# Performance work log

Measured on AMD Instinct MI355X. Metric: run time of the kernel, lower is better.

## Reference

```python
import jax, jax.numpy as jnp
import numpy as np

L, H, NH, KVH, HD, F, P, DLM, N = 4, 1024, 16, 2, 64, 4096, 4, 2048, 8192
QLEN = P + 1  # patch_size + 1 (special token prepended)
EPS = 1e-5


def _rms(x, w):
    return x * jax.lax.rsqrt(jnp.mean(x * x, axis=-1, keepdims=True) + EPS) * w


def _rotate_half(x):
    x1, x2 = jnp.split(x, 2, axis=-1)  # split_size = head_dim // 2
    return jnp.concatenate([-x2, x1], axis=-1)


def _rope_tables():
    pos = jnp.arange(QLEN, dtype=jnp.float32)
    inv_freq = 1.0 / (10000.0 ** (jnp.arange(0, HD, 2, dtype=jnp.float32) / HD))
    freqs = pos[:, None] * inv_freq[None, :]
    emb = jnp.concatenate([freqs, freqs], axis=-1)  # [QLEN, HD]
    scale = HD ** -0.25  # scale_factor baked into cos/sin as in source
    return jnp.cos(emb) * scale, jnp.sin(emb) * scale


def setup_inputs() -> dict:
    key = jax.random.key(0)
    ks = jax.random.split(key, 12)
    s = 0.02
    return {
        "audio_feat": jax.random.normal(ks[0], (N, P, 64), jnp.float32),
        "special_token": jax.random.normal(ks[1], (H,), jnp.float32) * s,
        "in_proj_w": jax.random.normal(ks[2], (64, H), jnp.float32) * s,
        "ln1_w": jnp.ones((L, H), jnp.float32),
        "wq": jax.random.normal(ks[3], (L, H, NH * HD), jnp.float32) * s,
        "wk": jax.random.normal(ks[4], (L, H, KVH * HD), jnp.float32) * s,
        "wv": jax.random.normal(ks[5], (L, H, KVH * HD), jnp.float32) * s,
        "wo": jax.random.normal(ks[6], (L, NH * HD, H), jnp.float32) * s,
        "ln2_w": jnp.ones((L, H), jnp.float32),
        "w_gate": jax.random.normal(ks[7], (L, H, F), jnp.float32) * s,
        "w_up": jax.random.normal(ks[8], (L, H, F), jnp.float32) * s,
        "w_down": jax.random.normal(ks[9], (L, F, H), jnp.float32) * s,
        "final_norm_w": jnp.ones((H,), jnp.float32),
        "enc_to_lm_w": jax.random.normal(ks[10], (H, DLM), jnp.float32) * s,
    }


def reference(audio_feat, special_token, in_proj_w, ln1_w, wq, wk, wv, wo,
              ln2_w, w_gate, w_up, w_down, final_norm_w, enc_to_lm_w):
    n = audio_feat.shape[0]
    h = audio_feat @ in_proj_w  # [N, P, H]
    sp = jnp.broadcast_to(special_token, (n, 1, H))
    h = jnp.concatenate([sp, h], axis=1)  # [N, QLEN, H]
    cos, sin = _rope_tables()
    g = NH // KVH  # num_key_value_groups
    for l in range(L):
        x = _rms(h, ln1_w[l])
        q = (x @ wq[l]).reshape(n, QLEN, NH, HD).transpose(0, 2, 1, 3)
        k = (x @ wk[l]).reshape(n, QLEN, KVH, HD).transpose(0, 2, 1, 3)
        v = (x @ wv[l]).reshape(n, QLEN, KVH, HD).transpose(0, 2, 1, 3)
        q = q * cos + _rotate_half(q) * sin
        k = k * cos + _rotate_half(k) * sin
        # explicit GQA repeat (cat-then-view == repeat along head axis)
        k = jnp.repeat(k, g, axis=1)
        v = jnp.repeat(v, g, axis=1)
        attn = jax.nn.softmax(jnp.einsum('bhqd,bhkd->bhqk', q, k), axis=-1)
        ao = jnp.einsum('bhqk,bhkd->bhqd', attn, v)
        ao = ao.transpose(0, 2, 1, 3).reshape(n, QLEN, NH * HD)
        h = h + ao @ wo[l]
        r = h
        x = _rms(h, ln2_w[l])
        h = r + (jax.nn.silu(x @ w_gate[l]) * (x @ w_up[l])) @ w_down[l]
    feat = _rms(h[:, 0], final_norm_w) @ enc_to_lm_w  # [N, DLM]
    return feat[None]  # [1, N, DLM]
```

## Files before the change

### kernel.cpp

```cpp
#include <hip/hip_runtime.h>
#include <hip/hip_bf16.h>

#define NSAMP 8192
#define QL 5
#define MTOK (NSAMP*QL)

typedef __hip_bfloat16 bf16;
typedef __attribute__((ext_vector_type(8))) __bf16 bf16x8;
typedef __attribute__((ext_vector_type(8))) unsigned short u16x8;
typedef __attribute__((ext_vector_type(4))) float f32x4;

__device__ __forceinline__ float bfu2f(unsigned short u){ return __uint_as_float(((unsigned)u)<<16); }
__device__ __forceinline__ float bf2f(bf16 v){ return __bfloat162float(v); }
__device__ __forceinline__ bf16  f2bf(float v){ return __float2bfloat16(v); }
__device__ __forceinline__ unsigned short f2bfu(float v){
  __hip_bfloat16 b = __float2bfloat16(v);
  return __builtin_bit_cast(unsigned short, b);
}

__device__ __forceinline__ void gload16(const void* g, void* l){
  __builtin_amdgcn_global_load_lds(
      (const __attribute__((address_space(1))) unsigned int*)g,
      (__attribute__((address_space(3))) unsigned int*)l, 16, 0, 0);
}

__device__ __forceinline__ void transpose_body(const float* __restrict__ in,
                                               bf16* __restrict__ out,
                                               int K, int N, int nb, int kb, int rmap){
  __shared__ float tile[32][33];
  int tx = threadIdx.x, ty = threadIdx.y;
  #pragma unroll
  for (int j=0;j<4;j++)
    tile[ty+8*j][tx] = in[(size_t)(kb+ty+8*j)*N + nb+tx];
  __syncthreads();
  #pragma unroll
  for (int j=0;j<4;j++){
    int n = nb+ty+8*j;
    int R = (rmap==0) ? n : (((n>>4)<<5) + (n&15) + (rmap==2 ? 16 : 0));
    out[(size_t)R*K + kb+tx] = f2bf(tile[tx][ty+8*j]);
  }
}

__global__ __launch_bounds__(256) void k_transpose_cvt(const float* __restrict__ in,
                                                       bf16* __restrict__ out,
                                                       int K, int N){
  transpose_body(in, out, K, N, blockIdx.x*32, blockIdx.y*32, 0);
}

__global__ __launch_bounds__(256) void k_transpose_layer(
    const float* __restrict__ wq, const float* __restrict__ wk,
    const float* __restrict__ wv, const float* __restrict__ wo,
    const float* __restrict__ wg, const float* __restrict__ wu,
    const float* __restrict__ wd,
    bf16* __restrict__ wqkvT, bf16* __restrict__ woT,
    bf16* __restrict__ wguT, bf16* __restrict__ wdT){
  int id = blockIdx.x;
  const float* in; bf16* out; int K=1024, N=1024, nbx=32, rmap=0;
  if (id < 1024){ in=wq; out=wqkvT; }
  else if (id < 1152){ id-=1024; in=wk; out=wqkvT+(size_t)1024*1024; N=128; nbx=4; }
  else if (id < 1280){ id-=1152; in=wv; out=wqkvT+(size_t)1152*1024; N=128; nbx=4; }
  else if (id < 2304){ id-=1280; in=wo; out=woT; }
  else if (id < 6400){ id-=2304; in=wg; out=wguT; N=4096; nbx=128; rmap=1; }
  else if (id < 10496){ id-=6400; in=wu; out=wguT; N=4096; nbx=128; rmap=2; }
  else { id-=10496; in=wd; out=wdT; K=4096; N=1024; nbx=32; }
  transpose_body(in, out, K, N, (id % nbx)*32, (id / nbx)*32, rmap);
}

__global__ __launch_bounds__(256) void k_cvt_bf16(const float* __restrict__ in,
                                                  bf16* __restrict__ out, int n4){
  int i = blockIdx.x*blockDim.x + threadIdx.x;
  if (i < n4){
    float4 v = ((const float4*)in)[i];
    out[4*i+0]=f2bf(v.x); out[4*i+1]=f2bf(v.y);
    out[4*i+2]=f2bf(v.z); out[4*i+3]=f2bf(v.w);
  }
}

__global__ __launch_bounds__(256) void k_fill_special(const float* __restrict__ sp,
                                                      bf16* __restrict__ h){
  int i = blockIdx.x*blockDim.x + threadIdx.x;
  int n = i >> 10, c = i & 1023;
  h[(size_t)n*QL*1024 + c] = f2bf(sp[c]);
}

__global__ void k_rope_tab(float* __restrict__ ctab, float* __restrict__ stab){
  int i = threadIdx.x;
  int t = i >> 6, d = i & 63, j = d & 31;
  float invf = __expf(-((float)j/32.0f) * logf(10000.0f));
  float ang  = (float)t * invf;
  const float s = 0.35355339059327373f;
  ctab[i] = cosf(ang)*s;
  stab[i] = sinf(ang)*s;
}

__global__ __launch_bounds__(256) void k_rmsnorm(const bf16* __restrict__ in,
                                                 const float* __restrict__ w,
                                                 bf16* __restrict__ out,
                                                 int nrows, int in_stride){
  int row  = blockIdx.x*4 + (threadIdx.x>>6);
  int lane = threadIdx.x & 63;
  if (row >= nrows) return;
  const bf16* p = in + (size_t)row*in_stride;
  float f[16]; float ss = 0.f;
  #pragma unroll
  for (int i=0;i<2;i++){
    u16x8 v = *(const u16x8*)(p + i*512 + lane*8);
    #pragma unroll
    for (int j=0;j<8;j++){ float x = bfu2f(v[j]); f[i*8+j] = x; ss += x*x; }
  }
  #pragma unroll
  for (int off=32; off; off>>=1) ss += __shfl_xor(ss, off);
  float inv = rsqrtf(ss * (1.0f/1024.0f) + 1e-5f);
  const float4* w4 = (const float4*)w;
  bf16* op = out + (size_t)row*1024;
  #pragma unroll
  for (int i=0;i<2;i++){
    int c = i*512 + lane*8;
    float4 wa = w4[c/4], wb = w4[c/4 + 1];
    u16x8 o;
    o[0]=f2bfu(f[i*8+0]*inv*wa.x); o[1]=f2bfu(f[i*8+1]*inv*wa.y);
    o[2]=f2bfu(f[i*8+2]*inv*wa.z); o[3]=f2bfu(f[i*8+3]*inv*wa.w);
    o[4]=f2bfu(f[i*8+4]*inv*wb.x); o[5]=f2bfu(f[i*8+5]*inv*wb.y);
    o[6]=f2bfu(f[i*8+6]*inv*wb.z); o[7]=f2bfu(f[i*8+7]*inv*wb.w);
    *(u16x8*)(op + c) = o;
  }
}

__global__ __launch_bounds__(256) void k_addnorm(bf16* __restrict__ h,
                                                 const float* __restrict__ w,
                                                 const bf16* __restrict__ add,
                                                 bf16* __restrict__ out,
                                                 int nrows){
  int row  = blockIdx.x*4 + (threadIdx.x>>6);
  int lane = threadIdx.x & 63;
  if (row >= nrows) return;
  bf16* hp = h + (size_t)row*1024;
  const bf16* ap = add + (size_t)row*1024;
  float f[16]; float ss = 0.f;
  u16x8 hv[2], av[2];
  #pragma unroll
  for (int i=0;i<2;i++){
    hv[i] = *(const u16x8*)(hp + i*512 + lane*8);
    av[i] = *(const u16x8*)(ap + i*512 + lane*8);
  }
  #pragma unroll
  for (int i=0;i<2;i++)
    #pragma unroll
    for (int j=0;j<8;j++){
      float x = bfu2f(hv[i][j]) + bfu2f(av[i][j]);
      f[i*8+j] = x; ss += x*x;
    }
  #pragma unroll
  for (int i=0;i<2;i++){
    u16x8 o;
    #pragma unroll
    for (int j=0;j<8;j++) o[j] = f2bfu(f[i*8+j]);
    *(u16x8*)(hp + i*512 + lane*8) = o;
  }
  #pragma unroll
  for (int off=32; off; off>>=1) ss += __shfl_xor(ss, off);
  float inv = rsqrtf(ss * (1.0f/1024.0f) + 1e-5f);
  const float4* w4 = (const float4*)w;
  bf16* op = out + (size_t)row*1024;
  #pragma unroll
  for (int i=0;i<2;i++){
    int c = i*512 + lane*8;
    float4 wa = w4[c/4], wb = w4[c/4 + 1];
    u16x8 o;
    o[0]=f2bfu(f[i*8+0]*inv*wa.x); o[1]=f2bfu(f[i*8+1]*inv*wa.y);
    o[2]=f2bfu(f[i*8+2]*inv*wa.z); o[3]=f2bfu(f[i*8+3]*inv*wa.w);
    o[4]=f2bfu(f[i*8+4]*inv*wb.x); o[5]=f2bfu(f[i*8+5]*inv*wb.y);
    o[6]=f2bfu(f[i*8+6]*inv*wb.z); o[7]=f2bfu(f[i*8+7]*inv*wb.w);
    *(u16x8*)(op + c) = o;
  }
}

__global__ __launch_bounds__(256) void k_add(bf16* __restrict__ h,
                                             const bf16* __restrict__ d, int n8){
  int i = blockIdx.x*blockDim.x + threadIdx.x;
  if (i < n8){
    u16x8 a = *(const u16x8*)(h + (size_t)i*8);
    u16x8 b = *(const u16x8*)(d + (size_t)i*8);
    u16x8 o;
    #pragma unroll
    for (int j=0;j<8;j++) o[j] = f2bfu(bfu2f(a[j]) + bfu2f(b[j]));
    *(u16x8*)(h + (size_t)i*8) = o;
  }
}

template<int OUTMODE>
__device__ __forceinline__ void gemm256_impl(const bf16* __restrict__ A,
                                             const bf16* __restrict__ B,
                                             float* __restrict__ Cf,
                                             bf16* __restrict__ Cb,
                                             int M, int N, int K, int ldc){
  __shared__ bf16 lds[65536];
  char* ldsb = (char*)lds;
  const int tid  = threadIdx.x;
  const int wid  = tid >> 6, lane = tid & 63;
  const int wr   = wid >> 2, wc  = wid & 3;
  const int fr   = lane & 15, fq = lane >> 4;
  const int swz = (fr & 7) << 4;
  const int cs0 = (fq*16) ^ swz;
  const int cs1 = (fq*16 + 64) ^ swz;
  const int srcR = lane >> 3;
  const int srcC = ((lane & 7) ^ srcR) * 8;

  const int bm0 = blockIdx.x*256, bn0 = blockIdx.y*256;
  const bf16* gA = A + (size_t)bm0*K;
  const bf16* gB = B + (size_t)bn0*K;
  const int nt = K >> 6;

  const int aOff = (wr ? 16384 : 0);
  const int bOff = 32768 + ((wc>>1) ? 16384 : 0) + (wc&1)*8192;
  const char* aB0 = ldsb + aOff + fr*128 + cs0;
  const char* aB1 = ldsb + aOff + fr*128 + cs1;
  const char* bB0 = ldsb + bOff + fr*128 + cs0;
  const char* bB1 = ldsb + bOff + fr*128 + cs1;

  f32x4 acc[8][4] = {};
  bf16x8 aF[8][2], bF[4][2];

#define STAGE(p, t, h) {                                                        \
    const bf16* G_ = ((h) < 2) ? gA : gB;                                       \
    const int rb_ = ((h)&1) ? 128 : 0;                                          \
    const int k0_ = (t) << 6;                                                   \
    _Pragma("unroll")                                                           \
    for (int j_=0;j_<2;j_++){                                                   \
      int blk_ = j_*8 + wid;                                                    \
      gload16(G_ + (size_t)(rb_ + blk_*8 + srcR)*K + k0_ + srcC,               \
              ldsb + (p)*65536 + (h)*16384 + blk_*1024);                        \
    }                                                                           \
  }
#define RD_A(p, m0_) {                                                          \
    _Pragma("unroll")                                                           \
    for (int m_=0;m_<4;m_++)                                                    \
      _Pragma("unroll")                                                         \
      for (int ks_=0;ks_<2;ks_++)                                               \
        aF[(m0_)+m_][ks_] = *(const bf16x8*)((ks_ ? aB1 : aB0) + (p)*65536 + ((m0_)+m_)*2048); \
  }
#define RD_B(p, n0_) {                                                          \
    _Pragma("unroll")                                                           \
    for (int n_=0;n_<2;n_++)                                                    \
      _Pragma("unroll")                                                         \
      for (int ks_=0;ks_<2;ks_++)                                               \
        bF[(n0_)+n_][ks_] = *(const bf16x8*)((ks_ ? bB1 : bB0) + (p)*65536 + ((n0_)+n_)*2048); \
  }
#define MM(qm_, qn_) {                                                          \
    _Pragma("unroll")                                                           \
    for (int m_=0;m_<4;m_++)                                                    \
      _Pragma("unroll")                                                         \
      for (int n_=0;n_<2;n_++)                                                  \
        _Pragma("unroll")                                                       \
        for (int ks_=0;ks_<2;ks_++)                                             \
          acc[(qm_)*4+m_][(qn_)*2+n_] = __builtin_amdgcn_mfma_f32_16x16x32_bf16( \
              aF[(qm_)*4+m_][ks_], bF[(qn_)*2+n_][ks_], acc[(qm_)*4+m_][(qn_)*2+n_], 0,0,0); \
  }
#define LGKM0  asm volatile("s_waitcnt lgkmcnt(0)" ::: "memory"); __builtin_amdgcn_sched_barrier(0)
#define BAR    __builtin_amdgcn_s_barrier()

  STAGE(0, 0, 0); STAGE(0, 0, 1); STAGE(0, 0, 2); STAGE(0, 0, 3);
  if (nt > 1){ STAGE(1, 1, 0); STAGE(1, 1, 1); STAGE(1, 1, 2); STAGE(1, 1, 3); }
  if (nt > 1) asm volatile("s_waitcnt vmcnt(8)" ::: "memory");
  else        asm volatile("s_waitcnt vmcnt(0)" ::: "memory");
  BAR;

  for (int t = 0; t < nt; t++){
    const int cur = t & 1;
    const bool pf = (t + 2) < nt;
    RD_A(cur, 0); RD_B(cur, 0);
    BAR; LGKM0;
    __builtin_amdgcn_s_setprio(1); MM(0,0); __builtin_amdgcn_s_setprio(0);
    BAR;
    RD_A(cur, 4);
    BAR; LGKM0;
    __builtin_amdgcn_s_setprio(1); MM(1,0); __builtin_amdgcn_s_setprio(0);
    BAR;
    RD_B(cur, 2);
    if (pf) STAGE(cur, t+2, 0);
    BAR; LGKM0;
    __builtin_amdgcn_s_setprio(1); MM(0,1); __builtin_amdgcn_s_setprio(0);
    BAR;
    if (pf){ STAGE(cur, t+2, 1); STAGE(cur, t+2, 2); STAGE(cur, t+2, 3); }
    BAR;
    __builtin_amdgcn_s_setprio(1); MM(1,1); __builtin_amdgcn_s_setprio(0);
    if (t + 1 < nt){
      if (pf) asm volatile("s_waitcnt vmcnt(8)" ::: "memory");
      else    asm volatile("s_waitcnt vmcnt(0)" ::: "memory");
    }
    BAR;
  }

  #pragma unroll
  for (int m=0;m<8;m++){
    if constexpr (OUTMODE == 2){
      #pragma unroll
      for (int n2=0;n2<2;n2++){
        #pragma unroll
        for (int i=0;i<4;i++){
          int row = bm0 + wr*128 + m*16 + fq*4 + i;
          int col = (bn0>>1) + wc*32 + n2*16 + fr;
          float g = acc[m][n2*2][i], u = acc[m][n2*2+1][i];
          Cb[(size_t)row*ldc + col] = f2bf((g / (1.0f + __expf(-g))) * u);
        }
      }
    } else {
      #pragma unroll
      for (int n=0;n<4;n++){
        #pragma unroll
        for (int i=0;i<4;i++){
          int row = bm0 + wr*128 + m*16 + fq*4 + i;
          int col = bn0 + wc*64 + n*16 + fr;
          size_t idx = (size_t)row*ldc + col;
          if constexpr (OUTMODE == 0) Cf[idx] = acc[m][n][i];
          else                        Cb[idx] = f2bf(acc[m][n][i]);
        }
      }
    }
  }
#undef STAGE
#undef RD_A
#undef RD_B
#undef MM
#undef LGKM0
#undef BAR
}

__global__ __launch_bounds__(512) void k_gemm_qkv(const bf16* A, const bf16* B, bf16* Cb, int M, int N, int K, int ldc){
  gemm256_impl<1>(A, B, nullptr, Cb, M, N, K, ldc);
}
__global__ __launch_bounds__(512) void k_gemm_wo(const bf16* A, const bf16* B, bf16* Cb, int M, int N, int K, int ldc){
  gemm256_impl<1>(A, B, nullptr, Cb, M, N, K, ldc);
}
__global__ __launch_bounds__(512) void k_gemm_gu(const bf16* A, const bf16* B, bf16* Cb, int M, int N, int K, int ldc){
  gemm256_impl<2>(A, B, nullptr, Cb, M, N, K, ldc);
}
__global__ __launch_bounds__(512) void k_gemm_down(const bf16* A, const bf16* B, bf16* Cb, int M, int N, int K, int ldc){
  gemm256_impl<1>(A, B, nullptr, Cb, M, N, K, ldc);
}
__global__ __launch_bounds__(512) void k_gemm_out(const bf16* A, const bf16* B, float* Cf, int M, int N, int K, int ldc){
  gemm256_impl<0>(A, B, Cf, nullptr, M, N, K, ldc);
}

__global__ __launch_bounds__(256) void k_gemm_embed(const bf16* __restrict__ A,
                                                    const bf16* __restrict__ B0,
                                                    bf16* __restrict__ Cb,
                                                    int M, int N, int K, int ldc){
  constexpr int BM = 128, BN = 128, BK = 32;
  constexpr int WN = BN/2, NR = WN/16, MR = 4;
  __shared__ bf16 lA[BM*BK];
  __shared__ bf16 lB[BN*BK];
  int wid = threadIdx.x >> 6, lane = threadIdx.x & 63;
  int wr = wid >> 1, wc = wid & 1;
  int bm0 = blockIdx.x * BM, bn0 = blockIdx.y * BN;
  int fr = lane & 15, fq = lane >> 4;
  int rowInCh = lane >> 2, colInCh = (lane & 3)*8;
  f32x4 acc[MR][NR] = {};
  const bf16* gA = A + (size_t)bm0*K;
  const bf16* gB = B0 + (size_t)bn0*K;
  for (int k0 = 0; k0 < K; k0 += BK){
    #pragma unroll
    for (int i = 0; i < BM/64; i++){
      int ch = wid + 4*i;
      gload16(gA + (size_t)(16*ch + rowInCh)*K + k0 + colInCh, lA + 16*ch*BK);
    }
    #pragma unroll
    for (int i = 0; i < BN/64; i++){
      int ch = wid + 4*i;
      gload16(gB + (size_t)(16*ch + rowInCh)*K + k0 + colInCh, lB + 16*ch*BK);
    }
    __syncthreads();
    bf16x8 af[MR];
    #pragma unroll
    for (int m=0;m<MR;m++)
      af[m] = *(const bf16x8*)(lA + (wr*64 + m*16 + fr)*BK + fq*8);
    #pragma unroll
    for (int n=0;n<NR;n++){
      bf16x8 bfr = *(const bf16x8*)(lB + (wc*WN + n*16 + fr)*BK + fq*8);
      #pragma unroll
      for (int m=0;m<MR;m++)
        acc[m][n] = __builtin_amdgcn_mfma_f32_16x16x32_bf16(af[m], bfr, acc[m][n], 0,0,0);
    }
    __syncthreads();
  }
  #pragma unroll
  for (int m=0;m<MR;m++)
    #pragma unroll
    for (int n=0;n<NR;n++)
      #pragma unroll
      for (int i=0;i<4;i++){
        int row = bm0 + wr*64 + m*16 + fq*4 + i;
        int col = bn0 + wc*WN + n*16 + fr;
        size_t orow = (size_t)(row + (row>>2) + 1);
        Cb[orow*(size_t)ldc + col] = f2bf(acc[m][n][i]);
      }
}

__global__ __launch_bounds__(256) void k_attn(const bf16* __restrict__ qkv,
                                              bf16* __restrict__ xn,
                                              const float* __restrict__ ctab,
                                              const float* __restrict__ stab){
  int gw   = blockIdx.x*4 + (threadIdx.x>>6);
  int lane = threadIdx.x & 63;
  int sample = gw >> 4, head = gw & 15, kvh = head >> 3;

  float qf[QL], kf[QL], vf[QL];
  #pragma unroll
  for (int t=0;t<QL;t++){
    size_t r = (size_t)(sample*QL + t)*1280;
    qf[t] = bf2f(qkv[r + head*64 + lane]);
    kf[t] = bf2f(qkv[r + 1024 + kvh*64 + lane]);
    vf[t] = bf2f(qkv[r + 1152 + kvh*64 + lane]);
  }
  #pragma unroll
  for (int t=0;t<QL;t++){
    float c = ctab[t*64+lane], s = stab[t*64+lane];
    float qo = __shfl_xor(qf[t], 32);
    float ko = __shfl_xor(kf[t], 32);
    float rq = (lane < 32) ? -qo : qo;
    float rk = (lane < 32) ? -ko : ko;
    qf[t] = qf[t]*c + rq*s;
    kf[t] = kf[t]*c + rk*s;
  }
  float p[QL][QL];
  #pragma unroll
  for (int i=0;i<QL;i++)
    #pragma unroll
    for (int j=0;j<QL;j++) p[i][j] = qf[i]*kf[j];
  #pragma unroll
  for (int off=32; off; off>>=1){
    #pragma unroll
    for (int i=0;i<QL;i++)
      #pragma unroll
      for (int j=0;j<QL;j++) p[i][j] += __shfl_xor(p[i][j], off);
  }
  #pragma unroll
  for (int i=0;i<QL;i++){
    float mx = p[i][0];
    #pragma unroll
    for (int j=1;j<QL;j++) mx = fmaxf(mx, p[i][j]);
    float sum = 0.f;
    #pragma unroll
    for (int j=0;j<QL;j++){ p[i][j] = __expf(p[i][j]-mx); sum += p[i][j]; }
    float rs = 1.0f/sum;
    float o = 0.f;
    #pragma unroll
    for (int j=0;j<QL;j++) o += p[i][j]*vf[j];
    xn[((size_t)(sample*QL+i))*1024 + head*64 + lane] = f2bf(o*rs);
  }
}

__global__ void k_diag(float* out, float v){ out[0] = v; }

extern "C" void kernel_launch(void* const* d_in, const int* in_sizes, int n_in,
                              void* d_out, int out_size, void* d_ws, size_t ws_size,
                              hipStream_t stream){
  const float* audio = (const float*)d_in[0];
  const float* sp    = (const float*)d_in[1];
  const float* inpw  = (const float*)d_in[2];
  const float* ln1   = (const float*)d_in[3];
  const float* wq    = (const float*)d_in[4];
  const float* wk    = (const float*)d_in[5];
  const float* wv    = (const float*)d_in[6];
  const float* wo    = (const float*)d_in[7];
  const float* ln2   = (const float*)d_in[8];
  const float* wg    = (const float*)d_in[9];
  const float* wu    = (const float*)d_in[10];
  const float* wd    = (const float*)d_in[11];
  const float* fnw   = (const float*)d_in[12];
  const float* enc   = (const float*)d_in[13];
  float* out = (float*)d_out;
  char* ws = (char*)d_ws;

  size_t o_h=0,o_wqkv=0,o_wo=0,o_wgu=0,o_wd=0,o_ct=0,o_st=0,o_xn=0,o_u=0;
  size_t C = 0;
  const size_t tiers[3] = {2048, 1024, 512};
  for (int t=0;t<3;t++){
    size_t c = tiers[t], Rc = c*QL;
    size_t off = 0;
    auto al = [&](size_t b){ size_t o=off; off=(off+b+255)&~(size_t)255; return o; };
    o_h   = al((size_t)MTOK*1024*2);
    o_wqkv= al((size_t)1280*1024*2);
    o_wo  = al((size_t)1024*1024*2);
    o_wgu = al((size_t)8192*1024*2);
    o_wd  = al((size_t)1024*4096*2);
    o_ct  = al(QL*64*4);
    o_st  = al(QL*64*4);
    o_xn  = al(Rc*1024*2);
    size_t ub = Rc*4096*2;
    if ((size_t)NSAMP*1024*2 > ub) ub = (size_t)NSAMP*1024*2;
    o_u   = al(ub);
    if (off <= ws_size){ C = c; break; }
  }
  if (C == 0){ k_diag<<<1,1,0,stream>>>(out, (float)ws_size); return; }
  const size_t Rc = C*QL;

  bf16*  h     = (bf16*)(ws + o_h);
  bf16*  wqkvT = (bf16*)(ws + o_wqkv);
  bf16*  woT   = (bf16*)(ws + o_wo);
  bf16*  wguT  = (bf16*)(ws + o_wgu);
  bf16*  wdT   = (bf16*)(ws + o_wd);
  float* ctab  = (float*)(ws + o_ct);
  float* stab  = (float*)(ws + o_st);
  bf16*  xn    = (bf16*)(ws + o_xn);
  bf16*  ubuf  = (bf16*)(ws + o_u);
  bf16*  inprojT = wqkvT;
  bf16*  encT    = wguT;

  dim3 tb(32,8);
  k_rope_tab<<<1, 320, 0, stream>>>(ctab, stab);
  k_transpose_cvt<<<dim3(32, 2), tb, 0, stream>>>(inpw, inprojT, 64, 1024);
  k_cvt_bf16<<<(32768*64/4)/256, 256, 0, stream>>>(audio, ubuf, 32768*64/4);
  k_fill_special<<<NSAMP*1024/256, 256, 0, stream>>>(sp, h);
  k_gemm_embed<<<dim3(32768/128, 1024/128), 256, 0, stream>>>(
      ubuf, inprojT, h, 32768, 1024, 64, 1024);

  for (int l=0;l<4;l++){
    k_transpose_layer<<<14592, tb, 0, stream>>>(
        wq + (size_t)l*1024*1024, wk + (size_t)l*1024*128, wv + (size_t)l*1024*128,
        wo + (size_t)l*1024*1024, wg + (size_t)l*1024*4096, wu + (size_t)l*1024*4096,
        wd + (size_t)l*4096*1024, wqkvT, woT, wguT, wdT);

    for (size_t c0 = 0; c0 < NSAMP; c0 += C){
      size_t r0 = c0*QL;
      bf16* hc = h + r0*1024;
      k_rmsnorm<<<Rc/4, 256, 0, stream>>>(hc, ln1 + l*1024, xn, (int)Rc, 1024);
      k_gemm_qkv<<<dim3(Rc/256, 5), 512, 0, stream>>>(
          xn, wqkvT, ubuf, (int)Rc, 1280, 1024, 1280);
      k_attn<<<C*16/4, 256, 0, stream>>>(ubuf, xn, ctab, stab);
      k_gemm_wo<<<dim3(Rc/256, 4), 512, 0, stream>>>(
          xn, woT, ubuf, (int)Rc, 1024, 1024, 1024);
      k_addnorm<<<Rc/4, 256, 0, stream>>>(hc, ln2 + l*1024, ubuf, xn, (int)Rc);
      k_gemm_gu<<<dim3(Rc/256, 32), 512, 0, stream>>>(
          xn, wguT, ubuf, (int)Rc, 8192, 1024, 4096);
      k_gemm_down<<<dim3(Rc/256, 4), 512, 0, stream>>>(
          ubuf, wdT, xn, (int)Rc, 1024, 4096, 1024);
      k_add<<<(Rc*1024/8 + 255)/256, 256, 0, stream>>>(hc, xn, (int)(Rc*1024/8));
    }
  }

  k_transpose_cvt<<<dim3(64, 32), tb, 0, stream>>>(enc, encT, 1024, 2048);
  k_rmsnorm<<<NSAMP/4, 256, 0, stream>>>(h, fnw, ubuf, NSAMP, QL*1024);
  k_gemm_out<<<dim3(NSAMP/256, 2048/256), 512, 0, stream>>>(
      ubuf, encT, out, NSAMP, 2048, 1024, 2048);
}
```

Baseline: 7.082 ms.

## Split GEMM prefetch: stage A one tile ahead and B two tiles ahead

Reworks the double-buffered LDS pipeline in the shared 256-tile GEMM. A halves of the next K-tile are now issued into the other buffer at the start of each iteration. B halves are issued two tiles ahead into the current buffer once their fragments have been read. The MFMA quadrant order changes to (0,0),(0,1),(1,0),(1,1) so B is consumed earlier, and one fixed vmcnt(4) wait replaces the conditional waits. The aim is to spread global-to-LDS traffic more evenly across the compute phases and shorten stalls at tile boundaries. The cost is a shorter prefetch distance for A, which could expose more load latency.

Result: faster. 6.780 ms (-4.3%).

```diff
diff --git a/kernel.cpp b/kernel.cpp
--- a/kernel.cpp
+++ b/kernel.cpp
@@ -232,19 +232,33 @@
               ldsb + (p)*65536 + (h)*16384 + blk_*1024);                        \
     }                                                                           \
   }
-#define RD_A(p, m0_) {                                                          \
+#define RD_A01(p) {                                                             \
     _Pragma("unroll")                                                           \
     for (int m_=0;m_<4;m_++)                                                    \
       _Pragma("unroll")                                                         \
       for (int ks_=0;ks_<2;ks_++)                                               \
-        aF[(m0_)+m_][ks_] = *(const bf16x8*)((ks_ ? aB1 : aB0) + (p)*65536 + ((m0_)+m_)*2048); \
-  }
-#define RD_B(p, n0_) {                                                          \
+        aF[m_][ks_] = *(const bf16x8*)((ks_ ? aB1 : aB0) + (p)*65536 + m_*2048); \
+  }
+#define RD_A23(p) {                                                             \
+    _Pragma("unroll")                                                           \
+    for (int m_=4;m_<8;m_++)                                                    \
+      _Pragma("unroll")                                                         \
+      for (int ks_=0;ks_<2;ks_++)                                               \
+        aF[m_][ks_] = *(const bf16x8*)((ks_ ? aB1 : aB0) + (p)*65536 + m_*2048); \
+  }
+#define RD_B01(p) {                                                             \
     _Pragma("unroll")                                                           \
     for (int n_=0;n_<2;n_++)                                                    \
       _Pragma("unroll")                                                         \
       for (int ks_=0;ks_<2;ks_++)                                               \
-        bF[(n0_)+n_][ks_] = *(const bf16x8*)((ks_ ? bB1 : bB0) + (p)*65536 + ((n0_)+n_)*2048); \
+        bF[n_][ks_] = *(const bf16x8*)((ks_ ? bB1 : bB0) + (p)*65536 + n_*2048); \
+  }
+#define RD_B23(p) {                                                             \
+    _Pragma("unroll")                                                           \
+    for (int n_=2;n_<4;n_++)                                                    \
+      _Pragma("unroll")                                                         \
+      for (int ks_=0;ks_<2;ks_++)                                               \
+        bF[n_][ks_] = *(const bf16x8*)((ks_ ? bB1 : bB0) + (p)*65536 + n_*2048); \
   }
 #define MM(qm_, qn_) {                                                          \
     _Pragma("unroll")                                                           \
@@ -257,37 +271,35 @@
               aF[(qm_)*4+m_][ks_], bF[(qn_)*2+n_][ks_], acc[(qm_)*4+m_][(qn_)*2+n_], 0,0,0); \
   }
 #define LGKM0  asm volatile("s_waitcnt lgkmcnt(0)" ::: "memory"); __builtin_amdgcn_sched_barrier(0)
+#define SBAR   __builtin_amdgcn_sched_barrier(0)
 #define BAR    __builtin_amdgcn_s_barrier()
 
   STAGE(0, 0, 0); STAGE(0, 0, 1); STAGE(0, 0, 2); STAGE(0, 0, 3);
-  if (nt > 1){ STAGE(1, 1, 0); STAGE(1, 1, 1); STAGE(1, 1, 2); STAGE(1, 1, 3); }
-  if (nt > 1) asm volatile("s_waitcnt vmcnt(8)" ::: "memory");
-  else        asm volatile("s_waitcnt vmcnt(0)" ::: "memory");
+  if (nt > 1){ STAGE(1, 1, 2); STAGE(1, 1, 3); }
+  asm volatile("s_waitcnt vmcnt(4)" ::: "memory"); SBAR;
   BAR;
 
   for (int t = 0; t < nt; t++){
     const int cur = t & 1;
-    const bool pf = (t + 2) < nt;
-    RD_A(cur, 0); RD_B(cur, 0);
+    if (t + 1 < nt) STAGE(cur^1, t+1, 0);
+    RD_A01(cur); RD_B01(cur);
     BAR; LGKM0;
     __builtin_amdgcn_s_setprio(1); MM(0,0); __builtin_amdgcn_s_setprio(0);
     BAR;
-    RD_A(cur, 4);
+    if (t + 1 < nt) STAGE(cur^1, t+1, 1);
+    RD_B23(cur);
+    BAR; LGKM0;
+    __builtin_amdgcn_s_setprio(1); MM(0,1); __builtin_amdgcn_s_setprio(0);
+    BAR;
+    if (t + 2 < nt) STAGE(cur, t+2, 2);
+    RD_A23(cur);
     BAR; LGKM0;
     __builtin_amdgcn_s_setprio(1); MM(1,0); __builtin_amdgcn_s_setprio(0);
     BAR;
-    RD_B(cur, 2);
-    if (pf) STAGE(cur, t+2, 0);
-    BAR; LGKM0;
-    __builtin_amdgcn_s_setprio(1); MM(0,1); __builtin_amdgcn_s_setprio(0);
-    BAR;
-    if (pf){ STAGE(cur, t+2, 1); STAGE(cur, t+2, 2); STAGE(cur, t+2, 3); }
+    if (t + 2 < nt) STAGE(cur, t+2, 3);
     BAR;
     __builtin_amdgcn_s_setprio(1); MM(1,1); __builtin_amdgcn_s_setprio(0);
-    if (t + 1 < nt){
-      if (pf) asm volatile("s_waitcnt vmcnt(8)" ::: "memory");
-      else    asm volatile("s_waitcnt vmcnt(0)" ::: "memory");
-    }
+    asm volatile("s_waitcnt vmcnt(4)" ::: "memory"); SBAR;
     BAR;
   }
 
@@ -319,10 +331,13 @@
     }
   }
 #undef STAGE
-#undef RD_A
-#undef RD_B
+#undef RD_A01
+#undef RD_A23
+#undef RD_B01
+#undef RD_B23
 #undef MM
 #undef LGKM0
+#undef SBAR
 #undef BAR
 }
 
```
